# Optimization experiments

Measured on AMD Instinct MI355X. Metric: run time of the kernel, lower is better.

The kernel has to match this reference:

```python
import jax, jax.numpy as jnp
import numpy as np
from functools import partial

T, B, OBS, H, A = 512, 256, 128, 64, 16


def ste_sign(x):
    # forward: sign(x); backward: identity (straight-through estimator)
    return x + jax.lax.stop_gradient(jnp.sign(x) - x)


def setup_inputs() -> dict:
    key = jax.random.key(0)
    ks = jax.random.split(key, 20)
    def lin_w(k, fan_in, fan_out, std=1.0):
        return (jax.random.normal(k, (fan_out, fan_in), jnp.float32) * (std / np.sqrt(fan_in)))
    inp = {
        "x": jax.random.normal(ks[0], (T * B, OBS), jnp.float32),
        "gru_state": jnp.zeros((1, B, H), jnp.float32),
        "done": (jax.random.uniform(ks[1], (T * B,)) < 0.05).astype(jnp.float32),
        # GRU params (PyTorch layout: [3H, in], gate order r,z,n)
        "w_ih": lin_w(ks[2], OBS, 3 * H),
        "w_hh": lin_w(ks[3], H, 3 * H),
        "b_ih": jnp.zeros((3 * H,), jnp.float32),
        "b_hh": jnp.zeros((3 * H,), jnp.float32),
        # actor MLP: (H+OBS)->64->64->A
        "a_w1": lin_w(ks[4], H + OBS, 64), "a_b1": jnp.zeros((64,), jnp.float32),
        "a_w2": lin_w(ks[5], 64, 64),      "a_b2": jnp.zeros((64,), jnp.float32),
        "a_w3": lin_w(ks[6], 64, A, std=0.01), "a_b3": jnp.zeros((A,), jnp.float32),
        # critic MLP: (H+OBS)->64->64->1
        "c_w1": lin_w(ks[7], H + OBS, 64), "c_b1": jnp.zeros((64,), jnp.float32),
        "c_w2": lin_w(ks[8], 64, 64),      "c_b2": jnp.zeros((64,), jnp.float32),
        "c_w3": lin_w(ks[9], 64, 1),       "c_b3": jnp.zeros((1,), jnp.float32),
    }
    return inp


def _gru_scan(x, gru_state, done, w_ih, w_hh, b_ih, b_hh):
    # x: [T*B, OBS], gru_state: [1, B, H], done: [T*B]
    bsz = gru_state.shape[1]
    xs = x.reshape(-1, bsz, x.shape[-1])       # [T, B, OBS]
    ds = done.reshape(-1, bsz)                 # [T, B]
    # input-to-hidden gates for the whole sequence in one GEMM
    gi_all = jnp.einsum("tbi,gi->tbg", xs, w_ih) + b_ih   # [T, B, 3H]
    h0 = gru_state[0]                          # [B, H]

    def step(h, inputs):
        gi, d = inputs
        h = (1.0 - d)[:, None] * h             # done-masking of carried state
        gh = h @ w_hh.T + b_hh                 # [B, 3H]
        i_r, i_z, i_n = jnp.split(gi, 3, axis=-1)
        h_r, h_z, h_n = jnp.split(gh, 3, axis=-1)
        r = jax.nn.sigmoid(i_r + h_r)
        z = jax.nn.sigmoid(i_z + h_z)
        n = jnp.tanh(i_n + r * h_n)
        h_new = (1.0 - z) * n + z * h
        # quantized == 1: carried state is STE-sign quantized
        h_carry = ste_sign(h_new)
        out = ste_sign(h_new)                  # per-step output is also quantized
        return h_carry, out

    h_last, outs = jax.lax.scan(step, h0, (gi_all, ds))
    hidden = outs.reshape(-1, h0.shape[-1])    # [T*B, H]
    return hidden, h_last[None]                # [T*B, H], [1, B, H]


def _mlp(y, w1, b1, w2, b2, w3, b3):
    y = jnp.tanh(y @ w1.T + b1)
    y = jnp.tanh(y @ w2.T + b2)
    return y @ w3.T + b3


def reference(x, gru_state, done, w_ih, w_hh, b_ih, b_hh,
              a_w1, a_b1, a_w2, a_b2, a_w3, a_b3,
              c_w1, c_b1, c_w2, c_b2, c_w3, c_b3):
    hidden, new_state = _gru_scan(x, gru_state, done, w_ih, w_hh, b_ih, b_hh)
    cat = jnp.concatenate([hidden, x], axis=1)            # input_to_actor=True
    logits = _mlp(cat, a_w1, a_b1, a_w2, a_b2, a_w3, a_b3)
    value = _mlp(cat, c_w1, c_b1, c_w2, c_b2, c_w3, c_b3)
    return logits, value, new_state
```

## Files before the change

### kernel.cpp

```cpp
#include <hip/hip_runtime.h>
#include <math.h>

#define TT 512
#define BB 256
#define OBSZ 128
#define HH 64
#define G3 192
#define NROW (TT*BB)
#define SEGCAP 128

__device__ __forceinline__ float fast_rcp(float x) {
    return __builtin_amdgcn_rcpf(x);
}
__device__ __forceinline__ float tanh_fast(float x) {
    float xc = fminf(fmaxf(x, -20.0f), 20.0f);
    float e2 = __expf(2.0f * xc);
    return (e2 - 1.0f) * fast_rcp(e2 + 1.0f);
}

__global__ __launch_bounds__(64, 1)
void seg_build_kernel(const float* __restrict__ done,
                      unsigned int* __restrict__ segs, int* __restrict__ segcnt)
{
    const int b = blockIdx.x;
    const int l = threadIdx.x;
    __shared__ int starts[SEGCAP];
    __shared__ int scnt_s;

    unsigned int m = 0;
    #pragma unroll
    for (int k = 0; k < 8; ++k) {
        int t = l*8 + k;
        float d = done[(size_t)t*BB + b];
        if (t > 0 && d != 0.f) m |= (1u << k);
    }
    int cnt = __popc(m) + (l == 0 ? 1 : 0);
    int inc = cnt;
    for (int s = 1; s < 64; s <<= 1) {
        int v = __shfl_up(inc, s);
        if (l >= s) inc += v;
    }
    int total = __shfl(inc, 63);
    int w = inc - cnt;
    if (l == 0 && w < SEGCAP) starts[w++] = 0;
    #pragma unroll
    for (int k = 0; k < 8; ++k)
        if (m & (1u << k)) { if (w < SEGCAP) starts[w] = l*8 + k; ++w; }
    if (l == 0) scnt_s = (total < SEGCAP) ? total : SEGCAP;
    __syncthreads();

    const int n = scnt_s;
    for (int i = l; i < n; i += 64) {
        int t0 = starts[i];
        int t1 = (i+1 < n) ? starts[i+1] : TT;
        int li = t1 - t0;
        int rank = 0;
        for (int j = 0; j < n; ++j) {
            int s0 = starts[j];
            int s1 = (j+1 < n) ? starts[j+1] : TT;
            int lj = s1 - s0;
            rank += (int)((lj > li) || (lj == li && j < i));
        }
        segs[(size_t)b*SEGCAP + rank] = (unsigned int)t0 | ((unsigned int)li << 16);
    }
    if (l == 0) segcnt[b] = n;
}

__global__ __launch_bounds__(512, 6)
void seg_scan_kernel(const float* __restrict__ gi_ws, const float* __restrict__ h0,
                     const float* __restrict__ done,
                     const float* __restrict__ w_hh, const float* __restrict__ b_hh,
                     const unsigned int* __restrict__ segs, const int* __restrict__ segcnt,
                     signed char* __restrict__ hidden, float* __restrict__ state_out)
{
    const int b    = blockIdx.x;
    const int scnt = segcnt[b];
    const int si0  = blockIdx.y * 2;
    if (si0 >= scnt) return;

    __shared__ __align__(16) float ws[G3*68];
    __shared__ __align__(16) float hb[2][HH];
    __shared__ __align__(16) float srz[2][2*HH];
    __shared__ __align__(16) float shnb[2][HH];

    const int tid = threadIdx.x;
    #pragma unroll
    for (int i = 0; i < 6; ++i) {
        int idx = tid + i*512;
        int g = idx >> 4, k4 = idx & 15;
        *(float4*)&ws[g*68 + k4*4] = *(const float4*)&w_hh[g*HH + k4*4];
    }

    const int grp = tid >> 8;
    const int tau = tid & 255;
    const int si  = si0 + grp;

    int t0 = 0, len = 0;
    if (si < scnt) {
        unsigned int sg = segs[(size_t)b*SEGCAP + si];
        t0  = (int)(sg & 0xffffu);
        len = (int)(sg >> 16);
    }
    const int lmax = (int)(segs[(size_t)b*SEGCAP + si0] >> 16);

    const size_t gbase = (size_t)b*TT;

    float bh = 0.f, gp0 = 0.f, gp1 = 0.f;
    float gn0 = 0.f, gn1 = 0.f;
    if (tau < G3) {
        bh  = b_hh[tau];
        gp0 = gi_ws[(gbase + t0)*G3 + tau];
        if (len > 1) gp1 = gi_ws[(gbase + t0+1)*G3 + tau];
    } else {
        const int hl = tau - G3;
        float hi = 0.f;
        if (len > 0 && t0 == 0) {
            float d0 = done[b];
            hi = (1.0f - d0) * h0[b*HH + hl];
        }
        hb[grp][hl] = hi;
        gn0 = gi_ws[(gbase + t0)*G3 + 128 + hl];
        if (len > 1) gn1 = gi_ws[(gbase + t0+1)*G3 + 128 + hl];
    }
    __syncthreads();

    for (int tt = 0; tt < lmax; ++tt) {
        const int t = t0 + tt;
        if (tau < G3 && tt < len) {
            float gi = gp0;
            gp0 = gp1;
            if (tt+2 < len) gp1 = gi_ws[(gbase + t+2)*G3 + tau];
            int hvi = __float_as_int(hb[grp][tau & 63]);
            const float* wrow = &ws[tau*68];
            float a0=0.f, a1=0.f, a2=0.f, a3=0.f;
            #pragma unroll
            for (int j4 = 0; j4 < HH/4; ++j4) {
                float4 wv = *(const float4*)(wrow + j4*4);
                a0 = fmaf(__int_as_float(__builtin_amdgcn_readlane(hvi, 4*j4+0)), wv.x, a0);
                a1 = fmaf(__int_as_float(__builtin_amdgcn_readlane(hvi, 4*j4+1)), wv.y, a1);
                a2 = fmaf(__int_as_float(__builtin_amdgcn_readlane(hvi, 4*j4+2)), wv.z, a2);
                a3 = fmaf(__int_as_float(__builtin_amdgcn_readlane(hvi, 4*j4+3)), wv.w, a3);
            }
            float gh = bh + ((a0+a1)+(a2+a3));
            if (tau < 2*HH) srz[grp][tau] = gi + gh;
            else            shnb[grp][tau-2*HH] = gh;
        }
        __syncthreads();

        if (tau >= G3 && tt < len) {
            const int hl = tau - G3;
            float gin = gn0;
            gn0 = gn1;
            if (tt+2 < len) gn1 = gi_ws[(gbase + t+2)*G3 + 128 + hl];
            float sr = srz[grp][hl];
            float sz = srz[grp][HH + hl];
            float r = 1.0f / (1.0f + expf(-sr));
            float z = 1.0f / (1.0f + expf(-sz));
            float n = tanhf(gin + r * shnb[grp][hl]);
            float hm = hb[grp][hl];
            float hnew = (1.0f - z)*n + z*hm;
            float s = (hnew > 0.f) ? 1.f : ((hnew < 0.f) ? -1.f : 0.f);
            hidden[(size_t)(t*BB + b)*HH + hl] = (signed char)s;
            if (t == TT-1) state_out[b*HH + hl] = s;
            hb[grp][hl] = s;
        }
        __syncthreads();
    }
}

__global__ __launch_bounds__(256, 2)
void gi_proj_kernel(const float* __restrict__ x,
                    const float* __restrict__ w_ih, const float* __restrict__ b_ih,
                    float* __restrict__ gi_ws)
{
    __shared__ __align__(16) float ws[G3*68];
    const int tid  = threadIdx.x;
    const int q    = tid & 31;
    const int rp   = tid >> 5;
    const int rowb = blockIdx.x * 32;

    float bg[6];
    #pragma unroll
    for (int jj = 0; jj < 6; ++jj) bg[jj] = b_ih[q + 32*jj];

    float c0[6][4], c1[6][4], c2[6][4], c3[6][4];
    #pragma unroll
    for (int jj = 0; jj < 6; ++jj)
        #pragma unroll
        for (int r = 0; r < 4; ++r) { c0[jj][r]=0.f; c1[jj][r]=0.f; c2[jj][r]=0.f; c3[jj][r]=0.f; }

    #pragma unroll
    for (int half = 0; half < 2; ++half) {
        __syncthreads();
        #pragma unroll
        for (int i = 0; i < 12; ++i) {
            int idx = tid + i*256;
            int g = idx >> 4, k4 = idx & 15;
            *(float4*)&ws[g*68 + k4*4] =
                *(const float4*)&w_ih[(size_t)g*OBSZ + half*64 + k4*4];
        }
        __syncthreads();

        for (int kc = 0; kc < 8; ++kc) {
            float cv[4][8];
            #pragma unroll
            for (int r = 0; r < 4; ++r) {
                const float* xp = x + (size_t)(rowb + rp*4 + r)*OBSZ + half*64 + kc*8;
                float4 a = *(const float4*)xp;
                float4 c = *(const float4*)(xp + 4);
                cv[r][0]=a.x; cv[r][1]=a.y; cv[r][2]=a.z; cv[r][3]=a.w;
                cv[r][4]=c.x; cv[r][5]=c.y; cv[r][6]=c.z; cv[r][7]=c.w;
            }
            #pragma unroll
            for (int jj = 0; jj < 6; ++jj) {
                const float* wp = &ws[(q + 32*jj)*68 + kc*8];
                float4 w0 = *(const float4*)wp;
                float4 w1 = *(const float4*)(wp + 4);
                #pragma unroll
                for (int r = 0; r < 4; ++r) {
                    c0[jj][r] = fmaf(cv[r][0], w0.x, c0[jj][r]);
                    c1[jj][r] = fmaf(cv[r][1], w0.y, c1[jj][r]);
                    c2[jj][r] = fmaf(cv[r][2], w0.z, c2[jj][r]);
                    c3[jj][r] = fmaf(cv[r][3], w0.w, c3[jj][r]);
                    c0[jj][r] = fmaf(cv[r][4], w1.x, c0[jj][r]);
                    c1[jj][r] = fmaf(cv[r][5], w1.y, c1[jj][r]);
                    c2[jj][r] = fmaf(cv[r][6], w1.z, c2[jj][r]);
                    c3[jj][r] = fmaf(cv[r][7], w1.w, c3[jj][r]);
                }
            }
        }
    }

    #pragma unroll
    for (int r = 0; r < 4; ++r) {
        const int row = rowb + rp*4 + r;
        const size_t rowp = ((size_t)(row & (BB-1)) << 9) | (row >> 8);
        #pragma unroll
        for (int jj = 0; jj < 6; ++jj) {
            float o = bg[jj] + ((c0[jj][r]+c1[jj][r]) + (c2[jj][r]+c3[jj][r]));
            gi_ws[rowp*G3 + q + 32*jj] = o;
        }
    }
}

__global__ __launch_bounds__(256, 1)
void scan_kernel_fused(const float* __restrict__ x, const float* __restrict__ h0,
                       const float* __restrict__ done,
                       const float* __restrict__ w_ih, const float* __restrict__ w_hh,
                       const float* __restrict__ b_ih, const float* __restrict__ b_hh,
                       signed char* __restrict__ hidden, float* __restrict__ state_out)
{
    const int b   = blockIdx.x;
    const int tau = threadIdx.x;

    __shared__ __align__(16) float xb[2][OBSZ];
    __shared__ __align__(16) float hb[HH];
    __shared__ __align__(16) float srz[2*HH];
    __shared__ __align__(16) float sinb[HH];
    __shared__ __align__(16) float shnb[HH];

    float4 wi4[OBSZ/4];
    float4 wh4[HH/4];
    float bi = 0.f, bh = 0.f;
    if (tau < G3) {
        const float4* wip = (const float4*)(w_ih + tau*OBSZ);
        #pragma unroll
        for (int k4 = 0; k4 < OBSZ/4; ++k4) wi4[k4] = wip[k4];
        const float4* whp = (const float4*)(w_hh + tau*HH);
        #pragma unroll
        for (int j4 = 0; j4 < HH/4; ++j4) wh4[j4] = whp[j4];
        bi = b_ih[tau]; bh = b_hh[tau];
    } else {
        const int hl = tau - G3;
        const int k0 = hl*2;
        float2 v = *(const float2*)(x + (size_t)(0*BB + b)*OBSZ + k0);
        xb[0][k0] = v.x; xb[0][k0+1] = v.y;
        float d0 = done[0*BB + b];
        hb[hl] = (1.0f - d0) * h0[b*HH + hl];
    }
    __syncthreads();

    float dnext = 0.f;
    for (int t = 0; t < TT; ++t) {
        const int cur = t & 1, nxt = cur ^ 1;
        if (tau < G3) {
            const float4* hb4 = (const float4*)hb;
            float a0=0.f, a1=0.f, a2=0.f, a3=0.f;
            #pragma unroll
            for (int j4 = 0; j4 < HH/4; ++j4) {
                float4 hv = hb4[j4];
                a0 = fmaf(hv.x, wh4[j4].x, a0);
                a1 = fmaf(hv.y, wh4[j4].y, a1);
                a2 = fmaf(hv.z, wh4[j4].z, a2);
                a3 = fmaf(hv.w, wh4[j4].w, a3);
            }
            float gh = bh + ((a0+a1)+(a2+a3));
            const float4* xb4 = (const float4*)xb[cur];
            float g0=0.f, g1=0.f, g2=0.f, g3=0.f;
            #pragma unroll
            for (int k4 = 0; k4 < OBSZ/4; ++k4) {
                float4 xv = xb4[k4];
                g0 = fmaf(xv.x, wi4[k4].x, g0);
                g1 = fmaf(xv.y, wi4[k4].y, g1);
                g2 = fmaf(xv.z, wi4[k4].z, g2);
                g3 = fmaf(xv.w, wi4[k4].w, g3);
            }
            float gi = bi + ((g0+g1)+(g2+g3));
            if (tau < 2*HH) srz[tau] = gi + gh;
            else { sinb[tau-2*HH] = gi; shnb[tau-2*HH] = gh; }
        } else {
            const int hl = tau - G3;
            if (t+1 < TT) {
                const int k0 = hl*2;
                float2 xr = *(const float2*)(x + (size_t)((t+1)*BB + b)*OBSZ + k0);
                xb[nxt][k0] = xr.x; xb[nxt][k0+1] = xr.y;
                dnext = done[(t+1)*BB + b];
            }
        }
        __syncthreads();

        if (tau >= G3) {
            const int hl = tau - G3;
            float sr = srz[hl];
            float sz = srz[HH + hl];
            float r = 1.0f / (1.0f + expf(-sr));
            float z = 1.0f / (1.0f + expf(-sz));
            float n = tanhf(sinb[hl] + r * shnb[hl]);
            float hm = hb[hl];
            float hnew = (1.0f - z)*n + z*hm;
            float s = (hnew > 0.f) ? 1.f : ((hnew < 0.f) ? -1.f : 0.f);
            hidden[(size_t)(t*BB + b)*HH + hl] = (signed char)s;
            if (t == TT-1) state_out[b*HH + hl] = s;
            hb[hl] = (t+1 < TT && dnext != 0.f) ? 0.f : s;
        }
        __syncthreads();
    }
}

__global__ __launch_bounds__(256, 2)
void mlp_both_kernel(const signed char* __restrict__ hidden, const float* __restrict__ x,
                     const float* __restrict__ a_w1, const float* __restrict__ a_b1,
                     const float* __restrict__ a_w2, const float* __restrict__ a_b2,
                     const float* __restrict__ a_w3, const float* __restrict__ a_b3,
                     const float* __restrict__ c_w1, const float* __restrict__ c_b1,
                     const float* __restrict__ c_w2, const float* __restrict__ c_b2,
                     const float* __restrict__ c_w3, const float* __restrict__ c_b3,
                     float* __restrict__ logits, float* __restrict__ value)
{
    const int head = blockIdx.y;
    const float* w1 = head ? c_w1 : a_w1;
    const float* b1 = head ? c_b1 : a_b1;
    const float* w2 = head ? c_w2 : a_w2;
    const float* b2 = head ? c_b2 : a_b2;
    const float* w3 = head ? c_w3 : a_w3;
    const float* b3 = head ? c_b3 : a_b3;
    const int  nout = head ? 1 : 16;
    float* out      = head ? value : logits;

    __shared__ __align__(16) float wbuf[64*100];
    __shared__ __align__(16) float ybuf[128*68];
    const int tid = threadIdx.x;
    const int g   = tid >> 3;
    const int q   = tid & 7;

    float bv1[8], bv2[8];
    #pragma unroll
    for (int j = 0; j < 8; ++j) { bv1[j] = b1[q + 8*j]; bv2[j] = b2[q + 8*j]; }

    for (int chunk = 0; chunk < 2; ++chunk) {
        const int row0 = blockIdx.x*256 + chunk*128 + g*4;

        float acc[8][4];
        #pragma unroll
        for (int j = 0; j < 8; ++j)
            #pragma unroll
            for (int r = 0; r < 4; ++r) acc[j][r] = bv1[j];

        auto dot8 = [&](float (&cv)[4][8], int colbase) {
            #pragma unroll
            for (int j = 0; j < 8; ++j) {
                const float* wp = &wbuf[(q + 8*j)*100 + colbase];
                float4 w0 = *(const float4*)wp;
                float4 w1v = *(const float4*)(wp + 4);
                #pragma unroll
                for (int r = 0; r < 4; ++r) {
                    acc[j][r] = fmaf(cv[r][0], w0.x,  acc[j][r]);
                    acc[j][r] = fmaf(cv[r][1], w0.y,  acc[j][r]);
                    acc[j][r] = fmaf(cv[r][2], w0.z,  acc[j][r]);
                    acc[j][r] = fmaf(cv[r][3], w0.w,  acc[j][r]);
                    acc[j][r] = fmaf(cv[r][4], w1v.x, acc[j][r]);
                    acc[j][r] = fmaf(cv[r][5], w1v.y, acc[j][r]);
                    acc[j][r] = fmaf(cv[r][6], w1v.z, acc[j][r]);
                    acc[j][r] = fmaf(cv[r][7], w1v.w, acc[j][r]);
                }
            }
        };

        #pragma unroll
        for (int half = 0; half < 2; ++half) {
            __syncthreads();
            #pragma unroll
            for (int i = 0; i < 6; ++i) {
                int v = tid + i*256;
                int f = v / 24, k4 = v % 24;
                *(float4*)&wbuf[f*100 + k4*4] =
                    *(const float4*)&w1[f*G3 + half*96 + k4*4];
            }
            __syncthreads();

            if (half == 0) {
                for (int kc = 0; kc < 8; ++kc) {
                    float cv[4][8];
                    #pragma unroll
                    for (int r = 0; r < 4; ++r) {
                        uint2 hv = *(const uint2*)(hidden + (size_t)(row0+r)*HH + kc*8);
                        cv[r][0] = (float)(signed char)(hv.x);
                        cv[r][1] = (float)(signed char)(hv.x >> 8);
                        cv[r][2] = (float)(signed char)(hv.x >> 16);
                        cv[r][3] = (float)(signed char)(hv.x >> 24);
                        cv[r][4] = (float)(signed char)(hv.y);
                        cv[r][5] = (float)(signed char)(hv.y >> 8);
                        cv[r][6] = (float)(signed char)(hv.y >> 16);
                        cv[r][7] = (float)(signed char)(hv.y >> 24);
                    }
                    dot8(cv, kc*8);
                }
                for (int kc = 0; kc < 4; ++kc) {
                    float cv[4][8];
                    #pragma unroll
                    for (int r = 0; r < 4; ++r) {
                        const float* xp = x + (size_t)(row0+r)*OBSZ + kc*8;
                        float4 a = *(const float4*)xp;
                        float4 c = *(const float4*)(xp + 4);
                        cv[r][0]=a.x; cv[r][1]=a.y; cv[r][2]=a.z; cv[r][3]=a.w;
                        cv[r][4]=c.x; cv[r][5]=c.y; cv[r][6]=c.z; cv[r][7]=c.w;
                    }
                    dot8(cv, 64 + kc*8);
                }
            } else {
                for (int kc = 0; kc < 12; ++kc) {
                    float cv[4][8];
                    #pragma unroll
                    for (int r = 0; r < 4; ++r) {
                        const float* xp = x + (size_t)(row0+r)*OBSZ + 32 + kc*8;
                        float4 a = *(const float4*)xp;
                        float4 c = *(const float4*)(xp + 4);
                        cv[r][0]=a.x; cv[r][1]=a.y; cv[r][2]=a.z; cv[r][3]=a.w;
                        cv[r][4]=c.x; cv[r][5]=c.y; cv[r][6]=c.z; cv[r][7]=c.w;
                    }
                    dot8(cv, kc*8);
                }
            }
        }

        #pragma unroll
        for (int j = 0; j < 8; ++j)
            #pragma unroll
            for (int r = 0; r < 4; ++r)
                ybuf[(g*4+r)*68 + q + 8*j] = tanh_fast(acc[j][r]);
        __syncthreads();

        #pragma unroll
        for (int i = 0; i < 4; ++i) {
            int v = tid + i*256;
            int f = v >> 4, k4 = v & 15;
            *(float4*)&wbuf[f*68 + k4*4] = *(const float4*)&w2[f*HH + k4*4];
        }
        __syncthreads();

        float acc2[8][4];
        #pragma unroll
        for (int j = 0; j < 8; ++j)
            #pragma unroll
            for (int r = 0; r < 4; ++r) acc2[j][r] = bv2[j];

        for (int kc = 0; kc < 8; ++kc) {
            float cv[4][8];
            #pragma unroll
            for (int r = 0; r < 4; ++r) {
                const float* yp = &ybuf[(g*4+r)*68 + kc*8];
                float4 a = *(const float4*)yp;
                float4 c = *(const float4*)(yp + 4);
                cv[r][0]=a.x; cv[r][1]=a.y; cv[r][2]=a.z; cv[r][3]=a.w;
                cv[r][4]=c.x; cv[r][5]=c.y; cv[r][6]=c.z; cv[r][7]=c.w;
            }
            #pragma unroll
            for (int j = 0; j < 8; ++j) {
                const float* wp = &wbuf[(q + 8*j)*68 + kc*8];
                float4 w0 = *(const float4*)wp;
                float4 w1v = *(const float4*)(wp + 4);
                #pragma unroll
                for (int r = 0; r < 4; ++r) {
                    acc2[j][r] = fmaf(cv[r][0], w0.x,  acc2[j][r]);
                    acc2[j][r] = fmaf(cv[r][1], w0.y,  acc2[j][r]);
                    acc2[j][r] = fmaf(cv[r][2], w0.z,  acc2[j][r]);
                    acc2[j][r] = fmaf(cv[r][3], w0.w,  acc2[j][r]);
                    acc2[j][r] = fmaf(cv[r][4], w1v.x, acc2[j][r]);
                    acc2[j][r] = fmaf(cv[r][5], w1v.y, acc2[j][r]);
                    acc2[j][r] = fmaf(cv[r][6], w1v.z, acc2[j][r]);
                    acc2[j][r] = fmaf(cv[r][7], w1v.w, acc2[j][r]);
                }
            }
        }
        __syncthreads();

        #pragma unroll
        for (int j = 0; j < 8; ++j)
            #pragma unroll
            for (int r = 0; r < 4; ++r)
                ybuf[(g*4+r)*68 + q + 8*j] = tanh_fast(acc2[j][r]);
        if (tid < nout*16) {
            int f = tid >> 4, k4 = tid & 15;
            *(float4*)&wbuf[f*68 + k4*4] = *(const float4*)&w3[f*HH + k4*4];
        }
        __syncthreads();

        for (int oo = 0; oo < (nout + 7)/8; ++oo) {
            const int o = q + 8*oo;
            if (o < nout) {
                #pragma unroll
                for (int r = 0; r < 4; ++r) {
                    const float* yp = &ybuf[(g*4+r)*68];
                    const float* wp = &wbuf[o*68];
                    float s0=0.f, s1=0.f, s2=0.f, s3=0.f;
                    #pragma unroll
                    for (int k4 = 0; k4 < 16; ++k4) {
                        float4 yv = *(const float4*)(yp + k4*4);
                        float4 wv = *(const float4*)(wp + k4*4);
                        s0 = fmaf(yv.x, wv.x, s0);
                        s1 = fmaf(yv.y, wv.y, s1);
                        s2 = fmaf(yv.z, wv.z, s2);
                        s3 = fmaf(yv.w, wv.w, s3);
                    }
                    out[(size_t)(row0+r)*nout + o] = b3[o] + ((s0+s1)+(s2+s3));
                }
            }
        }
        __syncthreads();
    }
}

extern "C" void kernel_launch(void* const* d_in, const int* in_sizes, int n_in,
                              void* d_out, int out_size, void* d_ws, size_t ws_size,
                              hipStream_t stream) {
    const float* x     = (const float*)d_in[0];
    const float* h0    = (const float*)d_in[1];
    const float* done  = (const float*)d_in[2];
    const float* w_ih  = (const float*)d_in[3];
    const float* w_hh  = (const float*)d_in[4];
    const float* b_ih  = (const float*)d_in[5];
    const float* b_hh  = (const float*)d_in[6];
    const float* a_w1  = (const float*)d_in[7];
    const float* a_b1  = (const float*)d_in[8];
    const float* a_w2  = (const float*)d_in[9];
    const float* a_b2  = (const float*)d_in[10];
    const float* a_w3  = (const float*)d_in[11];
    const float* a_b3  = (const float*)d_in[12];
    const float* c_w1  = (const float*)d_in[13];
    const float* c_b1  = (const float*)d_in[14];
    const float* c_w2  = (const float*)d_in[15];
    const float* c_b2  = (const float*)d_in[16];
    const float* c_w3  = (const float*)d_in[17];
    const float* c_b3  = (const float*)d_in[18];

    float* out    = (float*)d_out;
    float* logits = out;
    float* value  = out + (size_t)NROW*16;
    float* state  = value + NROW;

    const size_t segs_bytes   = (size_t)BB * SEGCAP * sizeof(unsigned int);
    const size_t segcnt_bytes = (size_t)BB * sizeof(int);
    const size_t hidden_off   = segs_bytes + segcnt_bytes;
    const size_t hidden_bytes = (size_t)NROW * HH;
    const size_t gi_off       = hidden_off + hidden_bytes;
    const size_t gi_bytes     = (size_t)NROW * G3 * sizeof(float);

    if (ws_size >= gi_off + gi_bytes) {
        unsigned int* segs = (unsigned int*)d_ws;
        int* segcnt        = (int*)((char*)d_ws + segs_bytes);
        signed char* hidden = (signed char*)((char*)d_ws + hidden_off);
        float* gi_ws       = (float*)((char*)d_ws + gi_off);

        seg_build_kernel<<<BB, 64, 0, stream>>>(done, segs, segcnt);
        gi_proj_kernel<<<NROW/32, 256, 0, stream>>>(x, w_ih, b_ih, gi_ws);
        seg_scan_kernel<<<dim3(BB, SEGCAP/2), 512, 0, stream>>>(
            gi_ws, h0, done, w_hh, b_hh, segs, segcnt, hidden, state);
        mlp_both_kernel<<<dim3(512, 2), 256, 0, stream>>>(
            hidden, x, a_w1, a_b1, a_w2, a_b2, a_w3, a_b3,
            c_w1, c_b1, c_w2, c_b2, c_w3, c_b3, logits, value);
    } else {
        signed char* hidden = (signed char*)d_ws;
        scan_kernel_fused<<<BB, 256, 0, stream>>>(x, h0, done, w_ih, w_hh,
                                                  b_ih, b_hh, hidden, state);
        mlp_both_kernel<<<dim3(512, 2), 256, 0, stream>>>(
            hidden, x, a_w1, a_b1, a_w2, a_b2, a_w3, a_b3,
            c_w1, c_b1, c_w2, c_b2, c_w3, c_b3, logits, value);
    }
}
```

Baseline: 471.3 us.

## Process four GRU segments per block, pairing segments per thread

The segmented GRU scan kernel now handles four reset-delimited segments per block instead of two. Each of the 384 matvec threads computes the recurrent gate product for two segments from a single read of its shared-memory weight row. Each of the 128 gate threads applies the nonlinearities for two segments in sequence. This halves the grid in y and the per-segment weight-row reads from shared memory, in exchange for a longer serial chain per time step on the gate threads, plus register pressure and idle lanes when paired segments differ in length.

```diff
diff --git a/kernel.cpp b/kernel.cpp
--- a/kernel.cpp
+++ b/kernel.cpp
@@ -66,7 +66,7 @@
     if (l == 0) segcnt[b] = n;
 }
 
-__global__ __launch_bounds__(512, 6)
+__global__ __launch_bounds__(512, 4)
 void seg_scan_kernel(const float* __restrict__ gi_ws, const float* __restrict__ h0,
                      const float* __restrict__ done,
                      const float* __restrict__ w_hh, const float* __restrict__ b_hh,
@@ -75,13 +75,13 @@
 {
     const int b    = blockIdx.x;
     const int scnt = segcnt[b];
-    const int si0  = blockIdx.y * 2;
+    const int si0  = blockIdx.y * 4;
     if (si0 >= scnt) return;
 
     __shared__ __align__(16) float ws[G3*68];
-    __shared__ __align__(16) float hb[2][HH];
-    __shared__ __align__(16) float srz[2][2*HH];
-    __shared__ __align__(16) float shnb[2][HH];
+    __shared__ __align__(16) float hb[4][HH];
+    __shared__ __align__(16) float srz[4][2*HH];
+    __shared__ __align__(16) float shnb[4][HH];
 
     const int tid = threadIdx.x;
     #pragma unroll
@@ -91,80 +91,151 @@
         *(float4*)&ws[g*68 + k4*4] = *(const float4*)&w_hh[g*HH + k4*4];
     }
 
-    const int grp = tid >> 8;
-    const int tau = tid & 255;
-    const int si  = si0 + grp;
-
-    int t0 = 0, len = 0;
-    if (si < scnt) {
-        unsigned int sg = segs[(size_t)b*SEGCAP + si];
-        t0  = (int)(sg & 0xffffu);
-        len = (int)(sg >> 16);
-    }
-    const int lmax = (int)(segs[(size_t)b*SEGCAP + si0] >> 16);
-
     const size_t gbase = (size_t)b*TT;
 
-    float bh = 0.f, gp0 = 0.f, gp1 = 0.f;
-    float gn0 = 0.f, gn1 = 0.f;
-    if (tau < G3) {
-        bh  = b_hh[tau];
-        gp0 = gi_ws[(gbase + t0)*G3 + tau];
-        if (len > 1) gp1 = gi_ws[(gbase + t0+1)*G3 + tau];
+    int t0q[4], lenq[4];
+    #pragma unroll
+    for (int s = 0; s < 4; ++s) {
+        if (si0 + s < scnt) {
+            unsigned int sg = segs[(size_t)b*SEGCAP + si0 + s];
+            t0q[s]  = (int)(sg & 0xffffu);
+            lenq[s] = (int)(sg >> 16);
+        } else { t0q[s] = 0; lenq[s] = 0; }
+    }
+    const int lmax = lenq[0];
+
+    if (tid < 384) {
+        const int pg  = tid / 192;
+        const int tau = tid % 192;
+        const int s0  = 2*pg, s1 = 2*pg + 1;
+        const int t00 = t0q[s0], len0 = lenq[s0];
+        const int t01 = t0q[s1], len1 = lenq[s1];
+
+        const float bh = b_hh[tau];
+        const float* wrow = &ws[tau*68];
+
+        float gpA0 = 0.f, gpA1 = 0.f, gpB0 = 0.f, gpB1 = 0.f;
+        if (len0 > 0) {
+            gpA0 = gi_ws[(gbase + t00)*G3 + tau];
+            if (len0 > 1) gpA1 = gi_ws[(gbase + t00+1)*G3 + tau];
+        }
+        if (len1 > 0) {
+            gpB0 = gi_ws[(gbase + t01)*G3 + tau];
+            if (len1 > 1) gpB1 = gi_ws[(gbase + t01+1)*G3 + tau];
+        }
+        __syncthreads();
+
+        for (int tt = 0; tt < lmax; ++tt) {
+            const bool doA = (tt < len0), doB = (tt < len1);
+            if (doA) {
+                float giA = gpA0;
+                gpA0 = gpA1;
+                if (tt+2 < len0) gpA1 = gi_ws[(gbase + t00+tt+2)*G3 + tau];
+                int hviA = __float_as_int(hb[s0][tau & 63]);
+                int hviB = 0;
+                float giB = 0.f;
+                if (doB) {
+                    giB = gpB0;
+                    gpB0 = gpB1;
+                    if (tt+2 < len1) gpB1 = gi_ws[(gbase + t01+tt+2)*G3 + tau];
+                    hviB = __float_as_int(hb[s1][tau & 63]);
+                }
+                float a0=0.f, a1=0.f, a2=0.f, a3=0.f;
+                float c0=0.f, c1=0.f, c2=0.f, c3=0.f;
+                #pragma unroll
+                for (int j4 = 0; j4 < HH/4; ++j4) {
+                    float4 wv = *(const float4*)(wrow + j4*4);
+                    a0 = fmaf(__int_as_float(__builtin_amdgcn_readlane(hviA, 4*j4+0)), wv.x, a0);
+                    a1 = fmaf(__int_as_float(__builtin_amdgcn_readlane(hviA, 4*j4+1)), wv.y, a1);
+                    a2 = fmaf(__int_as_float(__builtin_amdgcn_readlane(hviA, 4*j4+2)), wv.z, a2);
+                    a3 = fmaf(__int_as_float(__builtin_amdgcn_readlane(hviA, 4*j4+3)), wv.w, a3);
+                    if (doB) {
+                        c0 = fmaf(__int_as_float(__builtin_amdgcn_readlane(hviB, 4*j4+0)), wv.x, c0);
+                        c1 = fmaf(__int_as_float(__builtin_amdgcn_readlane(hviB, 4*j4+1)), wv.y, c1);
+                        c2 = fmaf(__int_as_float(__builtin_amdgcn_readlane(hviB, 4*j4+2)), wv.z, c2);
+                        c3 = fmaf(__int_as_float(__builtin_amdgcn_readlane(hviB, 4*j4+3)), wv.w, c3);
+                    }
+                }
+                float ghA = bh + ((a0+a1)+(a2+a3));
+                if (tau < 2*HH) srz[s0][tau] = giA + ghA;
+                else            shnb[s0][tau-2*HH] = ghA;
+                if (doB) {
+                    float ghB = bh + ((c0+c1)+(c2+c3));
+                    if (tau < 2*HH) srz[s1][tau] = giB + ghB;
+                    else            shnb[s1][tau-2*HH] = ghB;
+                }
+            }
+            __syncthreads();
+            __syncthreads();
+        }
     } else {
-        const int hl = tau - G3;
-        float hi = 0.f;
-        if (len > 0 && t0 == 0) {
+        const int gw = (tid - 384) >> 6;
+        const int hl = tid & 63;
+        const int s0 = 2*gw, s1 = 2*gw + 1;
+        const int t00 = t0q[s0], len0 = lenq[s0];
+        const int t01 = t0q[s1], len1 = lenq[s1];
+
+        float hiA = 0.f, hiB = 0.f;
+        if (len0 > 0 && t00 == 0) {
             float d0 = done[b];
-            hi = (1.0f - d0) * h0[b*HH + hl];
-        }
-        hb[grp][hl] = hi;
-        gn0 = gi_ws[(gbase + t0)*G3 + 128 + hl];
-        if (len > 1) gn1 = gi_ws[(gbase + t0+1)*G3 + 128 + hl];
-    }
-    __syncthreads();
-
-    for (int tt = 0; tt < lmax; ++tt) {
-        const int t = t0 + tt;
-        if (tau < G3 && tt < len) {
-            float gi = gp0;
-            gp0 = gp1;
-            if (tt+2 < len) gp1 = gi_ws[(gbase + t+2)*G3 + tau];
-            int hvi = __float_as_int(hb[grp][tau & 63]);
-            const float* wrow = &ws[tau*68];
-            float a0=0.f, a1=0.f, a2=0.f, a3=0.f;
-            #pragma unroll
-            for (int j4 = 0; j4 < HH/4; ++j4) {
-                float4 wv = *(const float4*)(wrow + j4*4);
-                a0 = fmaf(__int_as_float(__builtin_amdgcn_readlane(hvi, 4*j4+0)), wv.x, a0);
-                a1 = fmaf(__int_as_float(__builtin_amdgcn_readlane(hvi, 4*j4+1)), wv.y, a1);
-                a2 = fmaf(__int_as_float(__builtin_amdgcn_readlane(hvi, 4*j4+2)), wv.z, a2);
-                a3 = fmaf(__int_as_float(__builtin_amdgcn_readlane(hvi, 4*j4+3)), wv.w, a3);
-            }
-            float gh = bh + ((a0+a1)+(a2+a3));
-            if (tau < 2*HH) srz[grp][tau] = gi + gh;
-            else            shnb[grp][tau-2*HH] = gh;
-        }
-        __syncthreads();
-
-        if (tau >= G3 && tt < len) {
-            const int hl = tau - G3;
-            float gin = gn0;
-            gn0 = gn1;
-            if (tt+2 < len) gn1 = gi_ws[(gbase + t+2)*G3 + 128 + hl];
-            float sr = srz[grp][hl];
-            float sz = srz[grp][HH + hl];
-            float r = 1.0f / (1.0f + expf(-sr));
-            float z = 1.0f / (1.0f + expf(-sz));
-            float n = tanhf(gin + r * shnb[grp][hl]);
-            float hm = hb[grp][hl];
-            float hnew = (1.0f - z)*n + z*hm;
-            float s = (hnew > 0.f) ? 1.f : ((hnew < 0.f) ? -1.f : 0.f);
-            hidden[(size_t)(t*BB + b)*HH + hl] = (signed char)s;
-            if (t == TT-1) state_out[b*HH + hl] = s;
-            hb[grp][hl] = s;
-        }
-        __syncthreads();
+            hiA = (1.0f - d0) * h0[b*HH + hl];
+        }
+        if (len1 > 0 && t01 == 0) {
+            float d0 = done[b];
+            hiB = (1.0f - d0) * h0[b*HH + hl];
+        }
+        hb[s0][hl] = hiA;
+        hb[s1][hl] = hiB;
+
+        float gnA0 = 0.f, gnA1 = 0.f, gnB0 = 0.f, gnB1 = 0.f;
+        if (len0 > 0) {
+            gnA0 = gi_ws[(gbase + t00)*G3 + 128 + hl];
+            if (len0 > 1) gnA1 = gi_ws[(gbase + t00+1)*G3 + 128 + hl];
+        }
+        if (len1 > 0) {
+            gnB0 = gi_ws[(gbase + t01)*G3 + 128 + hl];
+            if (len1 > 1) gnB1 = gi_ws[(gbase + t01+1)*G3 + 128 + hl];
+        }
+        __syncthreads();
+
+        for (int tt = 0; tt < lmax; ++tt) {
+            __syncthreads();
+            if (tt < len0) {
+                const int t = t00 + tt;
+                float gin = gnA0;
+                gnA0 = gnA1;
+                if (tt+2 < len0) gnA1 = gi_ws[(gbase + t+2)*G3 + 128 + hl];
+                float sr = srz[s0][hl];
+                float sz = srz[s0][HH + hl];
+                float r = 1.0f / (1.0f + expf(-sr));
+                float z = 1.0f / (1.0f + expf(-sz));
+                float n = tanhf(gin + r * shnb[s0][hl]);
+                float hm = hb[s0][hl];
+                float hnew = (1.0f - z)*n + z*hm;
+                float s = (hnew > 0.f) ? 1.f : ((hnew < 0.f) ? -1.f : 0.f);
+                hidden[(size_t)(t*BB + b)*HH + hl] = (signed char)s;
+                if (t == TT-1) state_out[b*HH + hl] = s;
+                hb[s0][hl] = s;
+            }
+            if (tt < len1) {
+                const int t = t01 + tt;
+                float gin = gnB0;
+                gnB0 = gnB1;
+                if (tt+2 < len1) gnB1 = gi_ws[(gbase + t+2)*G3 + 128 + hl];
+                float sr = srz[s1][hl];
+                float sz = srz[s1][HH + hl];
+                float r = 1.0f / (1.0f + expf(-sr));
+                float z = 1.0f / (1.0f + expf(-sz));
+                float n = tanhf(gin + r * shnb[s1][hl]);
+                float hm = hb[s1][hl];
+                float hnew = (1.0f - z)*n + z*hm;
+                float s = (hnew > 0.f) ? 1.f : ((hnew < 0.f) ? -1.f : 0.f);
+                hidden[(size_t)(t*BB + b)*HH + hl] = (signed char)s;
+                if (t == TT-1) state_out[b*HH + hl] = s;
+                hb[s1][hl] = s;
+            }
+            __syncthreads();
+        }
     }
 }
 
@@ -583,7 +654,7 @@
 
         seg_build_kernel<<<BB, 64, 0, stream>>>(done, segs, segcnt);
         gi_proj_kernel<<<NROW/32, 256, 0, stream>>>(x, w_ih, b_ih, gi_ws);
-        seg_scan_kernel<<<dim3(BB, SEGCAP/2), 512, 0, stream>>>(
+        seg_scan_kernel<<<dim3(BB, SEGCAP/4), 512, 0, stream>>>(
             gi_ws, h0, done, w_hh, b_hh, segs, segcnt, hidden, state);
         mlp_both_kernel<<<dim3(512, 2), 256, 0, stream>>>(
             hidden, x, a_w1, a_b1, a_w2, a_b2, a_w3, a_b3,
```

Result: slower. 529.9 us (+12.4%).
